# Performance work log

Measured on AMD Instinct MI355X. Metric: run time of the kernel, lower is better.

The kernel has to match this reference:

```python
import jax, jax.numpy as jnp
import numpy as np

L = 26   # num_labels
D = 128  # input_dim


def setup_inputs() -> dict:
    key = jax.random.key(0)
    k1, k2, k3 = jax.random.split(key, 3)
    feat_x = jax.random.normal(k1, (8192, 64, 128), dtype=jnp.float32)
    input_y = jax.random.randint(k2, (8192, 64), 0, L, dtype=jnp.int32)
    # flat params: [L*D emission weights | L*L transition weights]
    params = jax.random.normal(k3, (L * D + L * L,), dtype=jnp.float32) * 0.1
    return {"feat_x": feat_x, "input_y": input_y, "params": params}


def reference(feat_x, input_y, params):
    # Linear-chain CRF negative average log-likelihood:
    #   loss = -mean_b [ score(y_b, x_b) - logZ(x_b) ]
    W = params[: L * D].reshape(L, D)      # emission weights
    Tr = params[L * D :].reshape(L, L)     # transition scores Tr[y_t, y_{t+1}]

    em = jnp.einsum("btd,ld->btl", feat_x, W)  # [B, T, L] emission scores

    # gold path score
    em_score = jnp.take_along_axis(em, input_y[..., None], axis=2)[..., 0].sum(axis=1)  # [B]
    tr_score = Tr[input_y[:, :-1], input_y[:, 1:]].sum(axis=1)                           # [B]

    # partition function via forward algorithm (log-sum-exp DP over time)
    em_t = jnp.swapaxes(em, 0, 1)  # [T, B, L]

    def step(alpha, e_t):
        # alpha: [B, L] log forward messages
        alpha = jax.nn.logsumexp(alpha[:, :, None] + Tr[None, :, :], axis=1) + e_t
        return alpha, None

    alpha_T, _ = jax.lax.scan(step, em_t[0], em_t[1:])
    logZ = jax.nn.logsumexp(alpha_T, axis=1)  # [B]

    return -jnp.mean(em_score + tr_score - logZ)
```

## Files before the change

kernel.cpp:

```cpp
#include <hip/hip_runtime.h>
#include <hip/hip_fp16.h>
#include <hip/hip_bf16.h>

#define NL 26
#define ND 128
#define NT 64
#define NB 8192
#define NIPB 32
#define ITP 34

typedef __attribute__((ext_vector_type(8))) short bf16x8;
typedef __attribute__((ext_vector_type(4))) float f32x4;

__device__ __forceinline__ uint32_t pk_bf16(float lo, float hi) {
    uint32_t r;
    asm("v_cvt_pk_bf16_f32 %0, %1, %2" : "=v"(r) : "v"(lo), "v"(hi));
    return r;
}

__global__ __launch_bounds__(512, 2) void crf_fused(
    const float* __restrict__ X, const int* __restrict__ Y,
    const float* __restrict__ P, float* __restrict__ partials)
{
    __shared__ float TrS[NL * NL];
    __shared__ __half emT[NT][32][ITP];
    __shared__ alignas(16) uint32_t pScr[2][16][20];
    __shared__ float goldS[NIPB];
    __shared__ int ready[4];

    const int tid = threadIdx.x;
    if (tid < 4) ready[tid] = 0;
    if (tid < NIPB) goldS[tid] = 0.f;
    for (int k = tid; k < NL * NL; k += 512) TrS[k] = P[NL * ND + k];
    __syncthreads();

    const int warp = tid >> 6;
    const int lane = tid & 63;
    const int r16  = lane & 15;
    const int kq   = lane >> 4;
    const int item0 = blockIdx.x * NIPB;

    if (warp > 0) {
        bf16x8 Bf[2][4];
        #pragma unroll
        for (int h = 0; h < 2; ++h) {
            int n = r16 + 16 * h;
            #pragma unroll
            for (int kb = 0; kb < 4; ++kb) {
                float w[8];
                if (n < NL) {
                    const float4* wp = reinterpret_cast<const float4*>(P + n * ND + kb * 32 + kq * 8);
                    float4 w0 = wp[0], w1 = wp[1];
                    w[0]=w0.x; w[1]=w0.y; w[2]=w0.z; w[3]=w0.w;
                    w[4]=w1.x; w[5]=w1.y; w[6]=w1.z; w[7]=w1.w;
                } else {
                    #pragma unroll
                    for (int jj = 0; jj < 8; ++jj) w[jj] = 0.f;
                }
                union { uint32_t u[4]; bf16x8 v; } pk;
                pk.u[0] = pk_bf16(w[0], w[1]); pk.u[1] = pk_bf16(w[2], w[3]);
                pk.u[2] = pk_bf16(w[4], w[5]); pk.u[3] = pk_bf16(w[6], w[7]);
                Bf[h][kb] = pk.v;
            }
        }

        const float4* X4 = reinterpret_cast<const float4*>(X);
        const int ibeg = (warp <= 4) ? (warp - 1) * 5 : 20 + (warp - 5) * 4;
        const int cnt  = (warp <= 4) ? 5 : 4;
        const int ntile = 4 * cnt;

        auto tile_load = [&](int k, int s, float4 (*xa)[2]) {
            size_t row  = (size_t)(item0 + ibeg + k) * NT + s * 16 + r16;
            size_t base = row * 32 + kq * 2;
            #pragma unroll
            for (int kb = 0; kb < 4; ++kb) {
                xa[kb][0] = X4[base + kb * 8];
                xa[kb][1] = X4[base + kb * 8 + 1];
            }
        };
        auto tile_comp = [&](int k, int s, float4 (*xa)[2]) {
            int it = ibeg + k;
            f32x4 acc0 = {0.f,0.f,0.f,0.f}, acc1 = {0.f,0.f,0.f,0.f};
            #pragma unroll
            for (int kb = 0; kb < 4; ++kb) {
                union { uint32_t u[4]; bf16x8 v; } A;
                A.u[0] = pk_bf16(xa[kb][0].x, xa[kb][0].y);
                A.u[1] = pk_bf16(xa[kb][0].z, xa[kb][0].w);
                A.u[2] = pk_bf16(xa[kb][1].x, xa[kb][1].y);
                A.u[3] = pk_bf16(xa[kb][1].z, xa[kb][1].w);
                acc0 = __builtin_amdgcn_mfma_f32_16x16x32_bf16(A.v, Bf[0][kb], acc0, 0, 0, 0);
                acc1 = __builtin_amdgcn_mfma_f32_16x16x32_bf16(A.v, Bf[1][kb], acc1, 0, 0, 0);
            }
            #pragma unroll
            for (int q = 0; q < 4; ++q) {
                int t = s * 16 + kq * 4 + q;
                emT[t][r16][it]      = __float2half(__expf(acc0[q]) * 0.0625f);
                emT[t][r16 + 16][it] = __float2half(__expf(acc1[q]) * 0.0625f);
            }
            if (lane < 16) {
                const int* yrow = Y + (size_t)(item0 + it) * NT;
                int tg = s * 16 + lane;
                int yt = yrow[tg];
                float g = __logf(__half2float(emT[tg][yt][it]));
                if (tg < NT - 1) g += TrS[yt * NL + yrow[tg + 1]];
                #pragma unroll
                for (int mk = 8; mk >= 1; mk >>= 1) g += __shfl_xor(g, mk);
                if (lane == 0) goldS[it] += g;
            }
            if (k == cnt - 1) {
                __threadfence_block();
                if (lane == 0) atomicAdd(&ready[s], 1);
            }
        };

        float4 xaA[4][2], xaB[4][2];
        int kc = 0, sc = 0;
        tile_load(0, 0, xaA);
        #pragma unroll 1
        for (int li = 0; li < ntile; li += 2) {
            int kn = kc + 1, sn = sc;
            if (kn == cnt) { kn = 0; ++sn; }
            if (sn < 4) tile_load(kn, sn, xaB);
            tile_comp(kc, sc, xaA);
            kc = kn; sc = sn;

            kn = kc + 1; sn = sc;
            if (kn == cnt) { kn = 0; ++sn; }
            if (sn < 4) tile_load(kn, sn, xaA);
            tile_comp(kc, sc, xaB);
            kc = kn; sc = sn;
        }
        return;
    }

    bf16x8 Ef[2];
    #pragma unroll
    for (int h = 0; h < 2; ++h) {
        int n = r16 + 16 * h;
        union { uint32_t u[4]; bf16x8 v; } c;
        #pragma unroll
        for (int w = 0; w < 4; ++w) {
            int sl = kq * 4 + w;
            float lo = (n < NL) ? __expf(TrS[sl * NL + n]) : 0.f;
            float hi = (n < NL && sl + 16 < NL) ? __expf(TrS[(sl + 16) * NL + n]) : 0.f;
            c.u[w] = pk_bf16(lo, hi);
        }
        Ef[h] = c.v;
    }

    bf16x8 pfA, pfB;
    float M[2][4] = {{0.f,0.f,0.f,0.f},{0.f,0.f,0.f,0.f}};
    float pn0[2][4], pn1[2][4];
    const f32x4 zacc = {0.f, 0.f, 0.f, 0.f};

    #pragma unroll 1
    for (int s = 0; s < 4; ++s) {
        volatile int* rp = (volatile int*)&ready[s];
        while (*rp < 7) __builtin_amdgcn_s_sleep(8);
        __threadfence_block();

        int t = s * 16;
        if (s == 0) {
            union { uint32_t u[4]; bf16x8 v; } c;
            #pragma unroll
            for (int w = 0; w < 4; ++w) {
                int sl = kq * 4 + w;
                float lo = __half2float(emT[0][sl][r16]);
                float hi = (sl + 16 < NL) ? __half2float(emT[0][sl + 16][r16]) : 0.f;
                c.u[w] = pk_bf16(lo, hi);
            }
            pfA = c.v;
            #pragma unroll
            for (int w = 0; w < 4; ++w) {
                int sl = kq * 4 + w;
                float lo = __half2float(emT[0][sl][16 + r16]);
                float hi = (sl + 16 < NL) ? __half2float(emT[0][sl + 16][16 + r16]) : 0.f;
                c.u[w] = pk_bf16(lo, hi);
            }
            pfB = c.v;
            t = 1;
        }
        const int tend = s * 16 + 16;
        #pragma unroll 1
        for (; t < tend; ++t) {
            f32x4 dA0 = __builtin_amdgcn_mfma_f32_16x16x32_bf16(pfA, Ef[0], zacc, 0, 0, 0);
            f32x4 dA1 = __builtin_amdgcn_mfma_f32_16x16x32_bf16(pfA, Ef[1], zacc, 0, 0, 0);
            f32x4 dB0 = __builtin_amdgcn_mfma_f32_16x16x32_bf16(pfB, Ef[0], zacc, 0, 0, 0);
            f32x4 dB1 = __builtin_amdgcn_mfma_f32_16x16x32_bf16(pfB, Ef[1], zacc, 0, 0, 0);
            #pragma unroll
            for (int g = 0; g < 2; ++g) {
                const f32x4& d0 = g ? dB0 : dA0;
                const f32x4& d1 = g ? dB1 : dA1;
                const __half2* pe0p = reinterpret_cast<const __half2*>(&emT[t][r16][g * 16 + kq * 4]);
                const __half2* pe1p = reinterpret_cast<const __half2*>(&emT[t][r16 + 16][g * 16 + kq * 4]);
                __half2 pe0a = pe0p[0], pe0b = pe0p[1];
                __half2 pe1a = pe1p[0], pe1b = pe1p[1];
                pn0[g][0] = d0[0] * __low2float(pe0a);  pn0[g][1] = d0[1] * __high2float(pe0a);
                pn0[g][2] = d0[2] * __low2float(pe0b);  pn0[g][3] = d0[3] * __high2float(pe0b);
                pn1[g][0] = d1[0] * __low2float(pe1a);  pn1[g][1] = d1[1] * __high2float(pe1a);
                pn1[g][2] = d1[2] * __low2float(pe1b);  pn1[g][3] = d1[3] * __high2float(pe1b);

                if ((t & 3) == 0) {
                    #pragma unroll
                    for (int q = 0; q < 4; ++q) {
                        float m = fmaxf(pn0[g][q], pn1[g][q]);
                        m = fmaxf(m, __shfl_xor(m, 1));
                        m = fmaxf(m, __shfl_xor(m, 2));
                        m = fmaxf(m, __shfl_xor(m, 4));
                        m = fmaxf(m, __shfl_xor(m, 8));
                        float r = __builtin_amdgcn_rcpf(m);
                        pn0[g][q] *= r; pn1[g][q] *= r;
                        M[g][q] += __logf(m);
                    }
                }
                #pragma unroll
                for (int q = 0; q < 4; ++q)
                    pScr[g][kq * 4 + q][r16] = pk_bf16(pn0[g][q], pn1[g][q]);
            }
            uint4 pwA = *reinterpret_cast<const uint4*>(&pScr[0][r16][kq * 4]);
            uint4 pwB = *reinterpret_cast<const uint4*>(&pScr[1][r16][kq * 4]);
            union { uint4 u; bf16x8 v; } pc;
            pc.u = pwA; pfA = pc.v;
            pc.u = pwB; pfB = pc.v;
        }
    }

    float tot = 0.f;
    #pragma unroll
    for (int g = 0; g < 2; ++g) {
        #pragma unroll
        for (int q = 0; q < 4; ++q) {
            float ssum = pn0[g][q] + pn1[g][q];
            ssum += __shfl_xor(ssum, 1);
            ssum += __shfl_xor(ssum, 2);
            ssum += __shfl_xor(ssum, 4);
            ssum += __shfl_xor(ssum, 8);
            float logZ = M[g][q] + __logf(ssum);
            tot += goldS[g * 16 + kq * 4 + q] - logZ;
        }
    }
    tot += __shfl_xor(tot, 16);
    tot += __shfl_xor(tot, 32);
    if (lane == 0) partials[blockIdx.x] = tot;
}

__global__ void crf_reduce2(const float* __restrict__ partials,
                            float* __restrict__ out, int n) {
    __shared__ float red[256];
    float s = 0.f;
    for (int i = threadIdx.x; i < n; i += 256) s += partials[i];
    red[threadIdx.x] = s;
    __syncthreads();
    for (int k = 128; k >= 1; k >>= 1) {
        if ((int)threadIdx.x < k) red[threadIdx.x] += red[threadIdx.x + k];
        __syncthreads();
    }
    if (threadIdx.x == 0) out[0] = -red[0] / (float)NB;
}

extern "C" void kernel_launch(void* const* d_in, const int* in_sizes, int n_in,
                              void* d_out, int out_size, void* d_ws, size_t ws_size,
                              hipStream_t stream) {
    const float* X = (const float*)d_in[0];
    const int*   Y = (const int*)d_in[1];
    const float* P = (const float*)d_in[2];
    float* out = (float*)d_out;
    float* partials = (float*)d_ws;

    crf_fused<<<NB / NIPB, 512, 0, stream>>>(X, Y, P, partials);
    crf_reduce2<<<1, 256, 0, stream>>>(partials, out, NB / NIPB);
}
```

Baseline: 74.67 us.

## Reorder emission tiles time-major across warps and stage labels in LDS

The 128 emission tiles are split evenly across the 7 producer warps in time-major order, so every time-chunk stage is produced by all warps together. This lets the forward-recursion warp start on chunk 0 earlier instead of waiting for each warp's item-major sequence. The per-stage ready counter now counts individual tiles (32 per stage), and gold scores go into per-stage slots so no two warps add into the same value. Labels are also loaded once into LDS with coalesced int4 loads instead of per-lane global reads. The cost is one LDS atomic and fence per tile rather than per warp-stage, plus extra LDS space.

Result: slower. 80.93 us (+8.4%).

```diff
diff --git a/kernel.cpp b/kernel.cpp
--- a/kernel.cpp
+++ b/kernel.cpp
@@ -25,13 +25,17 @@
     __shared__ float TrS[NL * NL];
     __shared__ __half emT[NT][32][ITP];
     __shared__ alignas(16) uint32_t pScr[2][16][20];
-    __shared__ float goldS[NIPB];
+    __shared__ alignas(16) float goldS2[NIPB][4];
+    __shared__ alignas(16) int yS[NIPB][NT];
     __shared__ int ready[4];
 
     const int tid = threadIdx.x;
     if (tid < 4) ready[tid] = 0;
-    if (tid < NIPB) goldS[tid] = 0.f;
     for (int k = tid; k < NL * NL; k += 512) TrS[k] = P[NL * ND + k];
+    {
+        const int4* Y4 = reinterpret_cast<const int4*>(Y + (size_t)blockIdx.x * NIPB * NT);
+        reinterpret_cast<int4*>(&yS[0][0])[tid] = Y4[tid];
+    }
     __syncthreads();
 
     const int warp = tid >> 6;
@@ -65,12 +69,12 @@
         }
 
         const float4* X4 = reinterpret_cast<const float4*>(X);
-        const int ibeg = (warp <= 4) ? (warp - 1) * 5 : 20 + (warp - 5) * 4;
-        const int cnt  = (warp <= 4) ? 5 : 4;
-        const int ntile = 4 * cnt;
-
-        auto tile_load = [&](int k, int s, float4 (*xa)[2]) {
-            size_t row  = (size_t)(item0 + ibeg + k) * NT + s * 16 + r16;
+        const int g0 = ((warp - 1) * 128) / 7;
+        const int g1 = (warp * 128) / 7;
+
+        auto tile_load = [&](int g, float4 (*xa)[2]) {
+            int it = g & 31, s = g >> 5;
+            size_t row  = (size_t)(item0 + it) * NT + s * 16 + r16;
             size_t base = row * 32 + kq * 2;
             #pragma unroll
             for (int kb = 0; kb < 4; ++kb) {
@@ -78,8 +82,8 @@
                 xa[kb][1] = X4[base + kb * 8 + 1];
             }
         };
-        auto tile_comp = [&](int k, int s, float4 (*xa)[2]) {
-            int it = ibeg + k;
+        auto tile_comp = [&](int g, float4 (*xa)[2]) {
+            int it = g & 31, s = g >> 5;
             f32x4 acc0 = {0.f,0.f,0.f,0.f}, acc1 = {0.f,0.f,0.f,0.f};
             #pragma unroll
             for (int kb = 0; kb < 4; ++kb) {
@@ -98,38 +102,30 @@
                 emT[t][r16 + 16][it] = __float2half(__expf(acc1[q]) * 0.0625f);
             }
             if (lane < 16) {
-                const int* yrow = Y + (size_t)(item0 + it) * NT;
+                const int* yrow = yS[it];
                 int tg = s * 16 + lane;
                 int yt = yrow[tg];
-                float g = __logf(__half2float(emT[tg][yt][it]));
-                if (tg < NT - 1) g += TrS[yt * NL + yrow[tg + 1]];
+                float g2 = __logf(__half2float(emT[tg][yt][it]));
+                if (tg < NT - 1) g2 += TrS[yt * NL + yrow[tg + 1]];
                 #pragma unroll
-                for (int mk = 8; mk >= 1; mk >>= 1) g += __shfl_xor(g, mk);
-                if (lane == 0) goldS[it] += g;
-            }
-            if (k == cnt - 1) {
-                __threadfence_block();
-                if (lane == 0) atomicAdd(&ready[s], 1);
-            }
+                for (int mk = 8; mk >= 1; mk >>= 1) g2 += __shfl_xor(g2, mk);
+                if (lane == 0) goldS2[it][s] = g2;
+            }
+            __threadfence_block();
+            if (lane == 0) atomicAdd(&ready[s], 1);
         };
 
         float4 xaA[4][2], xaB[4][2];
-        int kc = 0, sc = 0;
-        tile_load(0, 0, xaA);
+        int g = g0;
+        tile_load(g, xaA);
         #pragma unroll 1
-        for (int li = 0; li < ntile; li += 2) {
-            int kn = kc + 1, sn = sc;
-            if (kn == cnt) { kn = 0; ++sn; }
-            if (sn < 4) tile_load(kn, sn, xaB);
-            tile_comp(kc, sc, xaA);
-            kc = kn; sc = sn;
-
-            kn = kc + 1; sn = sc;
-            if (kn == cnt) { kn = 0; ++sn; }
-            if (sn < 4) tile_load(kn, sn, xaA);
-            tile_comp(kc, sc, xaB);
-            kc = kn; sc = sn;
-        }
+        for (; g + 2 <= g1; g += 2) {
+            tile_load(g + 1, xaB);
+            tile_comp(g, xaA);
+            if (g + 2 < g1) tile_load(g + 2, xaA);
+            tile_comp(g + 1, xaB);
+        }
+        if (g < g1) tile_comp(g, xaA);
         return;
     }
 
@@ -156,7 +152,7 @@
     #pragma unroll 1
     for (int s = 0; s < 4; ++s) {
         volatile int* rp = (volatile int*)&ready[s];
-        while (*rp < 7) __builtin_amdgcn_s_sleep(8);
+        while (*rp < 32) __builtin_amdgcn_s_sleep(8);
         __threadfence_block();
 
         int t = s * 16;
@@ -236,7 +232,10 @@
             ssum += __shfl_xor(ssum, 4);
             ssum += __shfl_xor(ssum, 8);
             float logZ = M[g][q] + __logf(ssum);
-            tot += goldS[g * 16 + kq * 4 + q] - logZ;
+            int it = g * 16 + kq * 4 + q;
+            float4 gs = *reinterpret_cast<const float4*>(&goldS2[it][0]);
+            float gold = ((gs.x + gs.y) + (gs.z + gs.w));
+            tot += gold - logZ;
         }
     }
     tot += __shfl_xor(tot, 16);
```
